# Kernel tuning notes

Measured on AMD Instinct MI355X. Metric: run time of the kernel, lower is better.

The kernel has to match this reference:

```python
import jax, jax.numpy as jnp
import numpy as np

B, S, D, H = 2, 2048, 2048, 16
HD = D // H
SCALE = 1.0 / np.sqrt(HD)


def setup_inputs() -> dict:
    key = jax.random.key(0)
    ks = jax.random.split(key, 11)
    xav = np.sqrt(6.0 / (D + D))  # xavier uniform bound for square weights
    def w(k):
        return jax.random.uniform(k, (D, D), jnp.float32, -xav, xav)
    return {
        "query": jax.random.normal(ks[0], (B, S, D), jnp.float32),
        "key": jax.random.normal(ks[1], (B, S, D), jnp.float32),
        "value": jax.random.normal(ks[2], (B, S, D), jnp.float32),
        "Wq": w(ks[3]), "bq": jnp.zeros((D,), jnp.float32),
        "Wk": w(ks[4]), "bk": jnp.zeros((D,), jnp.float32),
        "Wv": w(ks[5]), "bv": jnp.zeros((D,), jnp.float32),
        "Wo": w(ks[6]), "bo": jnp.zeros((D,), jnp.float32),
    }


def reference(query, key, value, Wq, bq, Wk, bk, Wv, bv, Wo, bo):
    # projections (torch Linear: x @ W.T + b)
    q = query @ Wq.T + bq
    k = key @ Wk.T + bk
    v = value @ Wv.T + bv
    # [B, H, S, HD]
    q = q.reshape(B, S, H, HD).transpose(0, 2, 1, 3)
    k = k.reshape(B, S, H, HD).transpose(0, 2, 1, 3)
    v = v.reshape(B, S, H, HD).transpose(0, 2, 1, 3)
    scores = jnp.einsum("bhqd,bhkd->bhqk", q, k) * SCALE
    causal = jnp.triu(jnp.ones((S, S), bool), k=1)
    scores = jnp.where(causal, -jnp.inf, scores)
    attn = jax.nn.softmax(scores, axis=-1)  # dropout p=0.0 -> identity
    out = jnp.einsum("bhqk,bhkd->bhqd", attn, v)
    out = out.transpose(0, 2, 1, 3).reshape(B, S, D)
    return out @ Wo.T + bo
```

## Files before the change

### kernel.cpp

```cpp
#include <hip/hip_runtime.h>
#include <hip/hip_bf16.h>


#define LOG2E 1.44269504088896340736f

typedef __attribute__((ext_vector_type(8))) short short8;
typedef __attribute__((ext_vector_type(4))) short short4b;
typedef __attribute__((ext_vector_type(4))) float floatx4;

__device__ __forceinline__ short f2bf(float f) {
  unsigned int u = __builtin_bit_cast(unsigned int, f);
  u += 0x7FFFu + ((u >> 16) & 1u);
  return (short)(u >> 16);
}

__device__ __forceinline__ short4b pack4bf(float a, float b, float c, float d) {
  __hip_bfloat162 lo = __float22bfloat162_rn(float2{a, b});
  __hip_bfloat162 hi = __float22bfloat162_rn(float2{c, d});
  short4b r;
  r[0] = __builtin_bit_cast(short, lo.x); r[1] = __builtin_bit_cast(short, lo.y);
  r[2] = __builtin_bit_cast(short, hi.x); r[3] = __builtin_bit_cast(short, hi.y);
  return r;
}

__device__ __forceinline__ void gl_lds16(const void* g, void* l) {
  __builtin_amdgcn_global_load_lds(
      (const __attribute__((address_space(1))) unsigned int*)g,
      (__attribute__((address_space(3))) unsigned int*)l, 16, 0, 0);
}

__global__ __launch_bounds__(256) void cvt_k(
    const float* __restrict__ s0, const float* __restrict__ s1,
    const float* __restrict__ s2, const float* __restrict__ s3,
    unsigned short* __restrict__ d0, unsigned short* __restrict__ d1,
    unsigned short* __restrict__ d2, unsigned short* __restrict__ d3, int n)
{
  const float* s; unsigned short* d;
  switch (blockIdx.y) {
    case 0: s = s0; d = d0; break;
    case 1: s = s1; d = d1; break;
    case 2: s = s2; d = d2; break;
    default: s = s3; d = d3; break;
  }
  const int i = (blockIdx.x * 256 + threadIdx.x) * 8;
  if (i >= n) return;
  float4 a = *(const float4*)(s + i);
  float4 b = *(const float4*)(s + i + 4);
  short8 v = (short8){f2bf(a.x), f2bf(a.y), f2bf(a.z), f2bf(a.w),
                      f2bf(b.x), f2bf(b.y), f2bf(b.z), f2bf(b.w)};
  *(short8*)(d + i) = v;
}

template<bool OUT_BF16, bool VT_OUT>
__global__ __launch_bounds__(512, 1) void gemm8_k(
    const unsigned short* __restrict__ A, const unsigned short* __restrict__ Bt,
    const float* __restrict__ bias, void* __restrict__ Cptr,
    int M, int N, int K, float alpha)
{
  __shared__ __align__(16) unsigned short As[3][256 * 64];
  __shared__ __align__(16) unsigned short Bs[3][128 * 64];
  (void)M;

  const int tid  = threadIdx.x;
  const int lane = tid & 63;
  const int wave = tid >> 6;
  const int quad = lane >> 4;
  const int l16  = lane & 15;
  const int lx7  = l16 & 7;
  const int wm   = wave >> 1, wn = wave & 1;

  int bx, by;
  if (gridDim.x == 16 && gridDim.y == 16) {
    const int lin  = (int)(blockIdx.y * 16 + blockIdx.x);
    const int xcd  = lin & 7;
    const int slot = lin >> 3;
    bx = (xcd & 1) * 8 + (slot & 7);
    by = (xcd >> 1) * 4 + (slot >> 3);
  } else { bx = (int)blockIdx.x; by = (int)blockIdx.y; }
  const long bm  = (long)by * 256;
  const long bn  = (long)bx * 128;

  const unsigned short* gA[4]; int lAo[4];
  const unsigned short* gB[2]; int lBo[2];
#pragma unroll
  for (int j = 0; j < 4; ++j) {
    const int pa = ((j >> 1) * 16 + wave * 2 + (j & 1)) * 64 + lane;
    const int r = pa >> 3, cp = pa & 7, cs = cp ^ (r & 7);
    gA[j]  = A + (bm + r) * (long)K + cs * 8;
    lAo[j] = pa * 8;
  }
#pragma unroll
  for (int j = 0; j < 2; ++j) {
    const int pb = (wave * 2 + j) * 64 + lane;
    const int r = pb >> 3, cp = pb & 7, cs = cp ^ (r & 7);
    gB[j]  = Bt + (bn + r) * (long)K + cs * 8;
    lBo[j] = pb * 8;
  }

  floatx4 acc[4][4];
#pragma unroll
  for (int i = 0; i < 4; ++i)
#pragma unroll
    for (int j = 0; j < 4; ++j) acc[i][j] = (floatx4){0.f, 0.f, 0.f, 0.f};

  const int NT = K >> 6;

#pragma unroll
  for (int j = 0; j < 4; ++j) gl_lds16(gA[j], &As[0][lAo[j]]);
#pragma unroll
  for (int j = 0; j < 2; ++j) gl_lds16(gB[j], &Bs[0][lBo[j]]);
  if (NT > 1) {
#pragma unroll
    for (int j = 0; j < 4; ++j) gl_lds16(gA[j] + 64, &As[1][lAo[j]]);
#pragma unroll
    for (int j = 0; j < 2; ++j) gl_lds16(gB[j] + 64, &Bs[1][lBo[j]]);
    asm volatile("s_waitcnt vmcnt(6)" ::: "memory");
  } else {
    asm volatile("s_waitcnt vmcnt(0)" ::: "memory");
  }
  __builtin_amdgcn_s_barrier();

  int cur = 0;
  for (int t = 0; t < NT; ++t) {
    int nx2 = cur + 2; if (nx2 >= 3) nx2 -= 3;
    const long kk2 = (long)(t + 2) * 64;
    const bool st  = (t + 2) < NT;
    const unsigned short* Ab = As[cur];
    const unsigned short* Bb = Bs[cur];

    short8 af[4][2];
#pragma unroll
    for (int mt = 0; mt < 4; ++mt)
#pragma unroll
      for (int ks = 0; ks < 2; ++ks)
        af[mt][ks] = *(const short8*)&Ab[(wm * 64 + mt * 16 + l16) * 64 +
                                         (((ks * 4 + quad) ^ lx7) * 8)];

    short8 bf00 = *(const short8*)&Bb[(wn * 64 +  0 + l16) * 64 + (((0 + quad) ^ lx7) * 8)];
    short8 bf01 = *(const short8*)&Bb[(wn * 64 +  0 + l16) * 64 + (((4 + quad) ^ lx7) * 8)];
    short8 bf10 = *(const short8*)&Bb[(wn * 64 + 16 + l16) * 64 + (((0 + quad) ^ lx7) * 8)];
    short8 bf11 = *(const short8*)&Bb[(wn * 64 + 16 + l16) * 64 + (((4 + quad) ^ lx7) * 8)];
    if (st) { gl_lds16(gA[0] + kk2, &As[nx2][lAo[0]]);
              gl_lds16(gA[1] + kk2, &As[nx2][lAo[1]]);
              gl_lds16(gA[2] + kk2, &As[nx2][lAo[2]]); }
    __builtin_amdgcn_s_barrier();
    asm volatile("s_waitcnt lgkmcnt(0)");
    __builtin_amdgcn_s_setprio(1);
#pragma unroll
    for (int mt = 0; mt < 4; ++mt) {
      acc[mt][0] = __builtin_amdgcn_mfma_f32_16x16x32_bf16(af[mt][0], bf00, acc[mt][0], 0, 0, 0);
      acc[mt][0] = __builtin_amdgcn_mfma_f32_16x16x32_bf16(af[mt][1], bf01, acc[mt][0], 0, 0, 0);
      acc[mt][1] = __builtin_amdgcn_mfma_f32_16x16x32_bf16(af[mt][0], bf10, acc[mt][1], 0, 0, 0);
      acc[mt][1] = __builtin_amdgcn_mfma_f32_16x16x32_bf16(af[mt][1], bf11, acc[mt][1], 0, 0, 0);
    }
    __builtin_amdgcn_s_setprio(0);
    __builtin_amdgcn_s_barrier();

    bf00 = *(const short8*)&Bb[(wn * 64 + 32 + l16) * 64 + (((0 + quad) ^ lx7) * 8)];
    bf01 = *(const short8*)&Bb[(wn * 64 + 32 + l16) * 64 + (((4 + quad) ^ lx7) * 8)];
    bf10 = *(const short8*)&Bb[(wn * 64 + 48 + l16) * 64 + (((0 + quad) ^ lx7) * 8)];
    bf11 = *(const short8*)&Bb[(wn * 64 + 48 + l16) * 64 + (((4 + quad) ^ lx7) * 8)];
    if (st) { gl_lds16(gA[3] + kk2, &As[nx2][lAo[3]]);
              gl_lds16(gB[0] + kk2, &Bs[nx2][lBo[0]]);
              gl_lds16(gB[1] + kk2, &Bs[nx2][lBo[1]]); }
    __builtin_amdgcn_s_barrier();
    asm volatile("s_waitcnt lgkmcnt(0)");
    __builtin_amdgcn_s_setprio(1);
#pragma unroll
    for (int mt = 0; mt < 4; ++mt) {
      acc[mt][2] = __builtin_amdgcn_mfma_f32_16x16x32_bf16(af[mt][0], bf00, acc[mt][2], 0, 0, 0);
      acc[mt][2] = __builtin_amdgcn_mfma_f32_16x16x32_bf16(af[mt][1], bf01, acc[mt][2], 0, 0, 0);
      acc[mt][3] = __builtin_amdgcn_mfma_f32_16x16x32_bf16(af[mt][0], bf10, acc[mt][3], 0, 0, 0);
      acc[mt][3] = __builtin_amdgcn_mfma_f32_16x16x32_bf16(af[mt][1], bf11, acc[mt][3], 0, 0, 0);
    }
    __builtin_amdgcn_s_setprio(0);
    if (t + 1 < NT) {
      if (st) asm volatile("s_waitcnt vmcnt(6)" ::: "memory");
      else    asm volatile("s_waitcnt vmcnt(0)" ::: "memory");
    }
    __builtin_amdgcn_s_barrier();

    cur = cur + 1 >= 3 ? 0 : cur + 1;
  }

  if (VT_OUT) {
    __syncthreads();
    unsigned short* Ct = &As[0][0];
#pragma unroll
    for (int nt = 0; nt < 4; ++nt) {
      const int col_l = wn * 64 + nt * 16 + l16;
      const float bval = bias[bn + col_l];
#pragma unroll
      for (int mt = 0; mt < 4; ++mt) {
        const int row_l = wm * 64 + mt * 16 + quad * 4;
#pragma unroll
        for (int rg = 0; rg < 4; ++rg)
          Ct[col_l * 264 + row_l + rg] = (unsigned short)f2bf((acc[mt][nt][rg] + bval) * alpha);
      }
    }
    __syncthreads();
    const int b  = (int)(bm >> 11);
    const int s0 = (int)(bm & 2047);
    const int d   = tid >> 2;
    const int seg = tid & 3;
    unsigned short* dst = (unsigned short*)Cptr +
        ((long)(b * 16 + bx) * 128 + d) * 2048 + s0 + seg * 64;
    const unsigned short* src = &Ct[d * 264 + seg * 64];
#pragma unroll
    for (int c = 0; c < 8; ++c)
      *(uint4*)(dst + c * 8) = *(const uint4*)(src + c * 8);
  } else {
#pragma unroll
    for (int nt = 0; nt < 4; ++nt) {
      const long col = bn + wn * 64 + nt * 16 + l16;
      const float bval = bias[col];
#pragma unroll
      for (int mt = 0; mt < 4; ++mt) {
#pragma unroll
        for (int rg = 0; rg < 4; ++rg) {
          const long row = bm + wm * 64 + mt * 16 + quad * 4 + rg;
          const float v = (acc[mt][nt][rg] + bval) * alpha;
          if (OUT_BF16) ((unsigned short*)Cptr)[row * (long)N + col] = (unsigned short)f2bf(v);
          else          ((float*)Cptr)[row * (long)N + col] = v;
        }
      }
    }
  }
}

template<bool A_BF16, bool OUT_BF16, bool VT_OUT>
__global__ __launch_bounds__(256, 2) void gemm_bias_k(
    const void* __restrict__ Aptr, const float* __restrict__ Bt,
    const float* __restrict__ bias, void* __restrict__ Cptr,
    int M, int N, int K, float alpha)
{
  __shared__ __align__(16) unsigned short smem[128 * 136];
  unsigned short* As = smem;
  unsigned short* Bs = smem + 128 * 40;

  const int tid  = threadIdx.x;
  const int lane = tid & 63;
  const int wave = tid >> 6;
  const int quad = lane >> 4;
  const int l16  = lane & 15;
  const int wr   = wave >> 1, wc = wave & 1;
  const long bm  = (long)blockIdx.y * 128;
  const long bn  = (long)blockIdx.x * 128;

  floatx4 acc[4][4];
#pragma unroll
  for (int i = 0; i < 4; ++i)
#pragma unroll
    for (int j = 0; j < 4; ++j) acc[i][j] = (floatx4){0.f, 0.f, 0.f, 0.f};

  const int srow = tid >> 2;
  const int cc   = tid & 3;

  for (int k0 = 0; k0 < K; k0 += 32) {
    __syncthreads();
#pragma unroll
    for (int r = 0; r < 2; ++r) {
      const int row = srow + r * 64;
      short8 av, bv;
      if (A_BF16) {
        av = *(const short8*)((const unsigned short*)Aptr + (bm + row) * (long)K + k0 + cc * 8);
      } else {
        const float* ap = (const float*)Aptr + (bm + row) * (long)K + k0 + cc * 8;
        float4 f0 = *(const float4*)ap;
        float4 f1 = *(const float4*)(ap + 4);
        av = (short8){f2bf(f0.x), f2bf(f0.y), f2bf(f0.z), f2bf(f0.w),
                      f2bf(f1.x), f2bf(f1.y), f2bf(f1.z), f2bf(f1.w)};
      }
      {
        const float* bp = Bt + (bn + row) * (long)K + k0 + cc * 8;
        float4 g0 = *(const float4*)bp;
        float4 g1 = *(const float4*)(bp + 4);
        bv = (short8){f2bf(g0.x), f2bf(g0.y), f2bf(g0.z), f2bf(g0.w),
                      f2bf(g1.x), f2bf(g1.y), f2bf(g1.z), f2bf(g1.w)};
      }
      *(short8*)&As[row * 40 + cc * 8] = av;
      *(short8*)&Bs[row * 40 + cc * 8] = bv;
    }
    __syncthreads();

    short8 af[4], bf[4];
#pragma unroll
    for (int t = 0; t < 4; ++t) {
      af[t] = *(const short8*)&As[(wr * 64 + t * 16 + l16) * 40 + quad * 8];
      bf[t] = *(const short8*)&Bs[(wc * 64 + t * 16 + l16) * 40 + quad * 8];
    }
#pragma unroll
    for (int mt = 0; mt < 4; ++mt)
#pragma unroll
      for (int nt = 0; nt < 4; ++nt)
        acc[mt][nt] = __builtin_amdgcn_mfma_f32_16x16x32_bf16(af[mt], bf[nt], acc[mt][nt], 0, 0, 0);
  }

  if (VT_OUT) {
    __syncthreads();
    unsigned short* Ct = smem;
#pragma unroll
    for (int nt = 0; nt < 4; ++nt) {
      const long col = bn + wc * 64 + nt * 16 + l16;
      const float bval = bias[col];
      const int col_l = wc * 64 + nt * 16 + l16;
#pragma unroll
      for (int mt = 0; mt < 4; ++mt) {
        const int row_l = wr * 64 + mt * 16 + quad * 4;
#pragma unroll
        for (int rg = 0; rg < 4; ++rg)
          Ct[col_l * 136 + row_l + rg] = (unsigned short)f2bf((acc[mt][nt][rg] + bval) * alpha);
      }
    }
    __syncthreads();
    const int b  = (int)(bm >> 11);
    const int s0 = (int)(bm & 2047);
    const int r    = tid >> 1;
    const int half = tid & 1;
    unsigned short* dst = (unsigned short*)Cptr +
        ((long)(b * 16 + blockIdx.x) * 128 + r) * 2048 + s0 + half * 64;
    const unsigned short* src = &Ct[r * 136 + half * 64];
#pragma unroll
    for (int c = 0; c < 8; ++c)
      *(uint4*)(dst + c * 8) = *(const uint4*)(src + c * 8);
  } else {
#pragma unroll
    for (int nt = 0; nt < 4; ++nt) {
      const long col = bn + wc * 64 + nt * 16 + l16;
      const float bval = bias[col];
#pragma unroll
      for (int mt = 0; mt < 4; ++mt) {
#pragma unroll
        for (int rg = 0; rg < 4; ++rg) {
          const long row = bm + wr * 64 + mt * 16 + quad * 4 + rg;
          const float v = (acc[mt][nt][rg] + bval) * alpha;
          if (OUT_BF16) ((unsigned short*)Cptr)[row * (long)N + col] = (unsigned short)f2bf(v);
          else          ((float*)Cptr)[row * (long)N + col] = v;
        }
      }
    }
  }
}

__global__ __launch_bounds__(256, 2) void flash_attn_k(
    const unsigned short* __restrict__ Q,
    const unsigned short* __restrict__ Kp,
    const unsigned short* __restrict__ Vt,
    unsigned short* __restrict__ O)
{
  constexpr int S = 2048, D = 2048, HD = 128;
  constexpr int PS = 72;

  __shared__ __align__(16) unsigned short Ks[2][64 * 128];
  __shared__ __align__(16) unsigned short Vst[2][128 * 64];
  __shared__ __align__(16) unsigned short Ps[64 * PS];

  const int tid  = threadIdx.x;
  const int lane = tid & 63;
  const int w    = tid >> 6;
  const int quad = lane >> 4;
  const int l16  = lane & 15;
  const int lx7  = l16 & 7;

  const int bx  = blockIdx.x;
  const int by  = blockIdx.y;
  const int idx = by * 2 + (bx >> 3);
  const int bh  = (bx & 7) * 4 + (idx >> 4);
  const int qsel = idx & 15;

  const long headoff = (long)(bh >> 4) * S * D + (long)(bh & 15) * HD;
  const long vtoff   = (long)bh * HD * S;

  const unsigned short* gK[4]; int oK[4];
  const unsigned short* gV[4]; int oV[4];
#pragma unroll
  for (int i = 0; i < 4; ++i) {
    const int p = (w * 4 + i) * 64 + lane;
    { const int r = p >> 4, cp = p & 15, c = cp ^ (r & 7);
      gK[i] = Kp + headoff + (long)r * D + c * 8;  oK[i] = p * 8; }
    { const int r = p >> 3, cp = p & 7, c = cp ^ (r & 7);
      gV[i] = Vt + vtoff + (long)r * S + c * 8;    oV[i] = p * 8; }
  }

#pragma unroll 1
  for (int half = 0; half < 2; ++half) {
    const int qt = half ? (31 - qsel) : qsel;
    const int qbase = qt * 64;
    const int qrow  = qbase + w * 16 + l16;
    const int qloc  = w * 16 + l16;

    short8 aq[4];
    {
      const unsigned short* qp = Q + headoff + (long)qrow * D;
#pragma unroll
      for (int ks = 0; ks < 4; ++ks)
        aq[ks] = *(const short8*)(qp + ks * 32 + quad * 8);
    }

    floatx4 o_acc[8];
#pragma unroll
    for (int t = 0; t < 8; ++t) o_acc[t] = (floatx4){0.f, 0.f, 0.f, 0.f};
    float m_i = -INFINITY, l_i = 0.f;

#pragma unroll
    for (int i = 0; i < 4; ++i) gl_lds16(gK[i], &Ks[0][oK[i]]);
#pragma unroll
    for (int i = 0; i < 4; ++i) gl_lds16(gV[i], &Vst[0][oV[i]]);

    for (int kt = 0; kt <= qt; ++kt) {
      const int cur = kt & 1;
      const int kbase = kt * 64;
      if (kt < qt) {
        const long kb = (long)(kt + 1) * 64;
        const int nb = cur ^ 1;
#pragma unroll
        for (int i = 0; i < 4; ++i) gl_lds16(gK[i] + kb * D, &Ks[nb][oK[i]]);
#pragma unroll
        for (int i = 0; i < 4; ++i) gl_lds16(gV[i] + kb, &Vst[nb][oV[i]]);
        asm volatile("s_waitcnt vmcnt(8)" ::: "memory");
      } else {
        asm volatile("s_waitcnt vmcnt(0)" ::: "memory");
      }
      __builtin_amdgcn_s_barrier();

      const unsigned short* Kb = &Ks[cur][0];
      const unsigned short* Vb = &Vst[cur][0];

      floatx4 sc[4];
#pragma unroll
      for (int nt = 0; nt < 4; ++nt) sc[nt] = (floatx4){0.f, 0.f, 0.f, 0.f};
      __builtin_amdgcn_s_setprio(1);
#pragma unroll
      for (int nt = 0; nt < 4; ++nt) {
        const int krow = nt * 16 + l16;
#pragma unroll
        for (int ks = 0; ks < 4; ++ks) {
          const int cp = (ks * 4 + quad) ^ lx7;
          short8 kf = *(const short8*)&Kb[krow * 128 + cp * 8];
          sc[nt] = __builtin_amdgcn_mfma_f32_16x16x32_bf16(kf, aq[ks], sc[nt], 0, 0, 0);
        }
      }
      __builtin_amdgcn_s_setprio(0);

      float sv[4][4];
      float rmax = -INFINITY;
      if (kt == qt) {
        const int kg0 = kbase + quad * 4;
#pragma unroll
        for (int nt = 0; nt < 4; ++nt)
#pragma unroll
          for (int rg = 0; rg < 4; ++rg) {
            float v = sc[nt][rg];
            if (kg0 + nt * 16 + rg > qrow) v = -INFINITY;
            sv[nt][rg] = v;
            rmax = fmaxf(rmax, v);
          }
      } else {
#pragma unroll
        for (int nt = 0; nt < 4; ++nt)
#pragma unroll
          for (int rg = 0; rg < 4; ++rg) {
            sv[nt][rg] = sc[nt][rg];
            rmax = fmaxf(rmax, sc[nt][rg]);
          }
      }
      rmax = fmaxf(rmax, __shfl_xor(rmax, 16));
      rmax = fmaxf(rmax, __shfl_xor(rmax, 32));

      float al = 1.0f;
      if (__any(rmax > m_i + 8.0f)) {
        const float mn = fmaxf(m_i, rmax);
        al = exp2f(m_i - mn);
        m_i = mn;
#pragma unroll
        for (int t = 0; t < 8; ++t)
#pragma unroll
          for (int rg = 0; rg < 4; ++rg) o_acc[t][rg] *= al;
      }

      float rsum = 0.f;
#pragma unroll
      for (int nt = 0; nt < 4; ++nt) {
        float p0 = exp2f(sv[nt][0] - m_i), p1 = exp2f(sv[nt][1] - m_i);
        float p2 = exp2f(sv[nt][2] - m_i), p3 = exp2f(sv[nt][3] - m_i);
        rsum += (p0 + p1) + (p2 + p3);
        *(short4b*)&Ps[qloc * PS + nt * 16 + quad * 4] = pack4bf(p0, p1, p2, p3);
      }
      rsum += __shfl_xor(rsum, 16);
      rsum += __shfl_xor(rsum, 32);
      l_i = l_i * al + rsum;

      short8 pf[2];
#pragma unroll
      for (int ks = 0; ks < 2; ++ks)
        pf[ks] = *(const short8*)&Ps[qloc * PS + ks * 32 + quad * 8];

      __builtin_amdgcn_s_setprio(1);
#pragma unroll
      for (int t = 0; t < 8; ++t) {
        const int drow = t * 16 + l16;
#pragma unroll
        for (int ks = 0; ks < 2; ++ks) {
          const int cp = (ks * 4 + quad) ^ lx7;
          short8 vf = *(const short8*)&Vb[drow * 64 + cp * 8];
          o_acc[t] = __builtin_amdgcn_mfma_f32_16x16x32_bf16(vf, pf[ks], o_acc[t], 0, 0, 0);
        }
      }
      __builtin_amdgcn_s_setprio(0);
      __builtin_amdgcn_s_barrier();
    }

    const float rl = 1.0f / l_i;
    unsigned short* op = O + headoff + (long)qrow * D;
#pragma unroll
    for (int t = 0; t < 8; ++t) {
      *(short4b*)(op + t * 16 + quad * 4) =
          pack4bf(o_acc[t][0] * rl, o_acc[t][1] * rl, o_acc[t][2] * rl, o_acc[t][3] * rl);
    }
  }
}

extern "C" void kernel_launch(void* const* d_in, const int* in_sizes, int n_in,
                              void* d_out, int out_size, void* d_ws, size_t ws_size,
                              hipStream_t stream) {
  const float* query = (const float*)d_in[0];
  const float* key_  = (const float*)d_in[1];
  const float* value = (const float*)d_in[2];
  const float* Wq = (const float*)d_in[3];
  const float* bq = (const float*)d_in[4];
  const float* Wk = (const float*)d_in[5];
  const float* bk = (const float*)d_in[6];
  const float* Wv = (const float*)d_in[7];
  const float* bv = (const float*)d_in[8];
  const float* Wo = (const float*)d_in[9];
  const float* bo = (const float*)d_in[10];
  float* out = (float*)d_out;

  constexpr int Bz = 2, S = 2048, D = 2048;
  constexpr int M = Bz * S;
  constexpr long NELEM = (long)M * D;
  constexpr long WELEM = (long)D * D;

  const float qscale = 0.08838834764831845f * LOG2E;
  dim3 gridG(D / 128, M / 128);
  dim3 gridG8(D / 128, M / 256);

  const size_t need_full = (size_t)(6 * NELEM + 4 * WELEM) * 2;

  if (ws_size >= need_full) {
    unsigned short* Qp  = (unsigned short*)d_ws;
    unsigned short* Kp  = Qp + NELEM;
    unsigned short* Vt  = Kp + NELEM;
    unsigned short* Xq  = Vt + NELEM;
    unsigned short* Xk  = Xq + NELEM;
    unsigned short* Xv  = Xk + NELEM;
    unsigned short* Wqb = Xv + NELEM;
    unsigned short* Wkb = Wqb + WELEM;
    unsigned short* Wvb = Wkb + WELEM;
    unsigned short* Wob = Wvb + WELEM;
    unsigned short* Oa  = Xq;

    cvt_k<<<dim3(NELEM / (8 * 256), 3), 256, 0, stream>>>(
        query, key_, value, value, Xq, Xk, Xv, Xv, (int)NELEM);
    cvt_k<<<dim3(WELEM / (8 * 256), 4), 256, 0, stream>>>(
        Wq, Wk, Wv, Wo, Wqb, Wkb, Wvb, Wob, (int)WELEM);

    gemm8_k<true, false><<<gridG8, 512, 0, stream>>>(Xq, Wqb, bq, Qp, M, D, D, qscale);
    gemm8_k<true, false><<<gridG8, 512, 0, stream>>>(Xk, Wkb, bk, Kp, M, D, D, 1.0f);
    gemm8_k<true, true ><<<gridG8, 512, 0, stream>>>(Xv, Wvb, bv, Vt, M, D, D, 1.0f);

    flash_attn_k<<<dim3(16, 32), 256, 0, stream>>>(Qp, Kp, Vt, Oa);

    gemm8_k<false, false><<<gridG8, 512, 0, stream>>>(Oa, Wob, bo, out, M, D, D, 1.0f);
  } else {
    unsigned short* Qp = (unsigned short*)d_ws;
    unsigned short* Kp = Qp + NELEM;
    unsigned short* Vt = Kp + NELEM;
    unsigned short* Oa = Vt + NELEM;

    gemm_bias_k<false, true, false><<<gridG, 256, 0, stream>>>(query, Wq, bq, Qp, M, D, D, qscale);
    gemm_bias_k<false, true, false><<<gridG, 256, 0, stream>>>(key_,  Wk, bk, Kp, M, D, D, 1.0f);
    gemm_bias_k<false, true, true ><<<gridG, 256, 0, stream>>>(value, Wv, bv, Vt, M, D, D, 1.0f);

    flash_attn_k<<<dim3(16, 32), 256, 0, stream>>>(Qp, Kp, Vt, Oa);

    gemm_bias_k<true, false, false><<<gridG, 256, 0, stream>>>(Oa, Wo, bo, out, M, D, D, 1.0f);
  }
}
```

Before: 424.8 us.

## Merge conversion kernels, simplify GEMM k-loop, defer softmax row-sum reductions

The two fp32-to-bf16 conversion launches become a single seven-slice kernel, with activation slices looping four times per block. The GEMM main loop now issues all six async global-to-LDS loads up front, then all A and B fragment reads, then all 32 MFMAs under one barrier. The old loop split this into two half-phases with extra barriers and lgkmcnt waits. In flash attention, the cross-lane max shuffles run only when a rescale happens, and the row-sum shuffles move out of the loop to a single reduction at the end. This raises register pressure for B fragments and can weaken interleaving of LDS reads with MFMAs.

```diff
diff --git a/kernel.cpp b/kernel.cpp
--- a/kernel.cpp
+++ b/kernel.cpp
@@ -29,26 +29,37 @@
       (__attribute__((address_space(3))) unsigned int*)l, 16, 0, 0);
 }
 
-__global__ __launch_bounds__(256) void cvt_k(
+__global__ __launch_bounds__(256) void cvt7_k(
     const float* __restrict__ s0, const float* __restrict__ s1,
     const float* __restrict__ s2, const float* __restrict__ s3,
+    const float* __restrict__ s4, const float* __restrict__ s5,
+    const float* __restrict__ s6,
     unsigned short* __restrict__ d0, unsigned short* __restrict__ d1,
-    unsigned short* __restrict__ d2, unsigned short* __restrict__ d3, int n)
+    unsigned short* __restrict__ d2, unsigned short* __restrict__ d3,
+    unsigned short* __restrict__ d4, unsigned short* __restrict__ d5,
+    unsigned short* __restrict__ d6, int nAct, int nW)
 {
-  const float* s; unsigned short* d;
+  const float* s; unsigned short* d; int n, iters;
   switch (blockIdx.y) {
-    case 0: s = s0; d = d0; break;
-    case 1: s = s1; d = d1; break;
-    case 2: s = s2; d = d2; break;
-    default: s = s3; d = d3; break;
-  }
-  const int i = (blockIdx.x * 256 + threadIdx.x) * 8;
-  if (i >= n) return;
-  float4 a = *(const float4*)(s + i);
-  float4 b = *(const float4*)(s + i + 4);
-  short8 v = (short8){f2bf(a.x), f2bf(a.y), f2bf(a.z), f2bf(a.w),
-                      f2bf(b.x), f2bf(b.y), f2bf(b.z), f2bf(b.w)};
-  *(short8*)(d + i) = v;
+    case 0: s = s0; d = d0; n = nAct; iters = 4; break;
+    case 1: s = s1; d = d1; n = nAct; iters = 4; break;
+    case 2: s = s2; d = d2; n = nAct; iters = 4; break;
+    case 3: s = s3; d = d3; n = nW;   iters = 1; break;
+    case 4: s = s4; d = d4; n = nW;   iters = 1; break;
+    case 5: s = s5; d = d5; n = nW;   iters = 1; break;
+    default: s = s6; d = d6; n = nW;  iters = 1; break;
+  }
+#pragma unroll 1
+  for (int c = 0; c < iters; ++c) {
+    const long i = ((long)(blockIdx.x + c * 2048) * 256 + threadIdx.x) * 8;
+    if (i < n) {
+      float4 a = *(const float4*)(s + i);
+      float4 b = *(const float4*)(s + i + 4);
+      short8 v = (short8){f2bf(a.x), f2bf(a.y), f2bf(a.z), f2bf(a.w),
+                          f2bf(b.x), f2bf(b.y), f2bf(b.z), f2bf(b.w)};
+      *(short8*)(d + i) = v;
+    }
+  }
 }
 
 template<bool OUT_BF16, bool VT_OUT>
@@ -120,67 +131,55 @@
   }
   __builtin_amdgcn_s_barrier();
 
-  int cur = 0;
+  int cur3 = 0;
   for (int t = 0; t < NT; ++t) {
-    int nx2 = cur + 2; if (nx2 >= 3) nx2 -= 3;
+    int nx2 = cur3 + 2; if (nx2 >= 3) nx2 -= 3;
     const long kk2 = (long)(t + 2) * 64;
-    const bool st  = (t + 2) < NT;
-    const unsigned short* Ab = As[cur];
-    const unsigned short* Bb = Bs[cur];
-
-    short8 af[4][2];
+    const bool st2 = (t + 2) < NT;
+    const bool st1 = (t + 1) < NT;
+    const unsigned short* Ab = As[cur3];
+    const unsigned short* Bb = Bs[cur3];
+
+    if (st2) {
+      gl_lds16(gA[0] + kk2, &As[nx2][lAo[0]]);
+      gl_lds16(gA[1] + kk2, &As[nx2][lAo[1]]);
+      gl_lds16(gA[2] + kk2, &As[nx2][lAo[2]]);
+      gl_lds16(gA[3] + kk2, &As[nx2][lAo[3]]);
+      gl_lds16(gB[0] + kk2, &Bs[nx2][lBo[0]]);
+      gl_lds16(gB[1] + kk2, &Bs[nx2][lBo[1]]);
+    }
+
+    short8 af[4][2], bf[4][2];
 #pragma unroll
     for (int mt = 0; mt < 4; ++mt)
 #pragma unroll
       for (int ks = 0; ks < 2; ++ks)
         af[mt][ks] = *(const short8*)&Ab[(wm * 64 + mt * 16 + l16) * 64 +
                                          (((ks * 4 + quad) ^ lx7) * 8)];
-
-    short8 bf00 = *(const short8*)&Bb[(wn * 64 +  0 + l16) * 64 + (((0 + quad) ^ lx7) * 8)];
-    short8 bf01 = *(const short8*)&Bb[(wn * 64 +  0 + l16) * 64 + (((4 + quad) ^ lx7) * 8)];
-    short8 bf10 = *(const short8*)&Bb[(wn * 64 + 16 + l16) * 64 + (((0 + quad) ^ lx7) * 8)];
-    short8 bf11 = *(const short8*)&Bb[(wn * 64 + 16 + l16) * 64 + (((4 + quad) ^ lx7) * 8)];
-    if (st) { gl_lds16(gA[0] + kk2, &As[nx2][lAo[0]]);
-              gl_lds16(gA[1] + kk2, &As[nx2][lAo[1]]);
-              gl_lds16(gA[2] + kk2, &As[nx2][lAo[2]]); }
+#pragma unroll
+    for (int nt = 0; nt < 4; ++nt)
+#pragma unroll
+      for (int ks = 0; ks < 2; ++ks)
+        bf[nt][ks] = *(const short8*)&Bb[(wn * 64 + nt * 16 + l16) * 64 +
+                                         (((ks * 4 + quad) ^ lx7) * 8)];
+
+    __builtin_amdgcn_s_setprio(1);
+#pragma unroll
+    for (int nt = 0; nt < 4; ++nt)
+#pragma unroll
+      for (int mt = 0; mt < 4; ++mt) {
+        acc[mt][nt] = __builtin_amdgcn_mfma_f32_16x16x32_bf16(af[mt][0], bf[nt][0], acc[mt][nt], 0, 0, 0);
+        acc[mt][nt] = __builtin_amdgcn_mfma_f32_16x16x32_bf16(af[mt][1], bf[nt][1], acc[mt][nt], 0, 0, 0);
+      }
+    __builtin_amdgcn_s_setprio(0);
+
+    if (st1) {
+      if (st2) asm volatile("s_waitcnt vmcnt(6)" ::: "memory");
+      else     asm volatile("s_waitcnt vmcnt(0)" ::: "memory");
+    }
     __builtin_amdgcn_s_barrier();
-    asm volatile("s_waitcnt lgkmcnt(0)");
-    __builtin_amdgcn_s_setprio(1);
-#pragma unroll
-    for (int mt = 0; mt < 4; ++mt) {
-      acc[mt][0] = __builtin_amdgcn_mfma_f32_16x16x32_bf16(af[mt][0], bf00, acc[mt][0], 0, 0, 0);
-      acc[mt][0] = __builtin_amdgcn_mfma_f32_16x16x32_bf16(af[mt][1], bf01, acc[mt][0], 0, 0, 0);
-      acc[mt][1] = __builtin_amdgcn_mfma_f32_16x16x32_bf16(af[mt][0], bf10, acc[mt][1], 0, 0, 0);
-      acc[mt][1] = __builtin_amdgcn_mfma_f32_16x16x32_bf16(af[mt][1], bf11, acc[mt][1], 0, 0, 0);
-    }
-    __builtin_amdgcn_s_setprio(0);
-    __builtin_amdgcn_s_barrier();
-
-    bf00 = *(const short8*)&Bb[(wn * 64 + 32 + l16) * 64 + (((0 + quad) ^ lx7) * 8)];
-    bf01 = *(const short8*)&Bb[(wn * 64 + 32 + l16) * 64 + (((4 + quad) ^ lx7) * 8)];
-    bf10 = *(const short8*)&Bb[(wn * 64 + 48 + l16) * 64 + (((0 + quad) ^ lx7) * 8)];
-    bf11 = *(const short8*)&Bb[(wn * 64 + 48 + l16) * 64 + (((4 + quad) ^ lx7) * 8)];
-    if (st) { gl_lds16(gA[3] + kk2, &As[nx2][lAo[3]]);
-              gl_lds16(gB[0] + kk2, &Bs[nx2][lBo[0]]);
-              gl_lds16(gB[1] + kk2, &Bs[nx2][lBo[1]]); }
-    __builtin_amdgcn_s_barrier();
-    asm volatile("s_waitcnt lgkmcnt(0)");
-    __builtin_amdgcn_s_setprio(1);
-#pragma unroll
-    for (int mt = 0; mt < 4; ++mt) {
-      acc[mt][2] = __builtin_amdgcn_mfma_f32_16x16x32_bf16(af[mt][0], bf00, acc[mt][2], 0, 0, 0);
-      acc[mt][2] = __builtin_amdgcn_mfma_f32_16x16x32_bf16(af[mt][1], bf01, acc[mt][2], 0, 0, 0);
-      acc[mt][3] = __builtin_amdgcn_mfma_f32_16x16x32_bf16(af[mt][0], bf10, acc[mt][3], 0, 0, 0);
-      acc[mt][3] = __builtin_amdgcn_mfma_f32_16x16x32_bf16(af[mt][1], bf11, acc[mt][3], 0, 0, 0);
-    }
-    __builtin_amdgcn_s_setprio(0);
-    if (t + 1 < NT) {
-      if (st) asm volatile("s_waitcnt vmcnt(6)" ::: "memory");
-      else    asm volatile("s_waitcnt vmcnt(0)" ::: "memory");
-    }
-    __builtin_amdgcn_s_barrier();
-
-    cur = cur + 1 >= 3 ? 0 : cur + 1;
+
+    cur3 = cur3 + 1 >= 3 ? 0 : cur3 + 1;
   }
 
   if (VT_OUT) {
@@ -400,7 +399,8 @@
     floatx4 o_acc[8];
 #pragma unroll
     for (int t = 0; t < 8; ++t) o_acc[t] = (floatx4){0.f, 0.f, 0.f, 0.f};
-    float m_i = -INFINITY, l_i = 0.f;
+    float m_i = -INFINITY;
+    float l_p = 0.f;
 
 #pragma unroll
     for (int i = 0; i < 4; ++i) gl_lds16(gK[i], &Ks[0][oK[i]]);
@@ -443,7 +443,7 @@
       __builtin_amdgcn_s_setprio(0);
 
       float sv[4][4];
-      float rmax = -INFINITY;
+      float lmax = -INFINITY;
       if (kt == qt) {
         const int kg0 = kbase + quad * 4;
 #pragma unroll
@@ -453,7 +453,7 @@
             float v = sc[nt][rg];
             if (kg0 + nt * 16 + rg > qrow) v = -INFINITY;
             sv[nt][rg] = v;
-            rmax = fmaxf(rmax, v);
+            lmax = fmaxf(lmax, v);
           }
       } else {
 #pragma unroll
@@ -461,14 +461,14 @@
 #pragma unroll
           for (int rg = 0; rg < 4; ++rg) {
             sv[nt][rg] = sc[nt][rg];
-            rmax = fmaxf(rmax, sc[nt][rg]);
+            lmax = fmaxf(lmax, sc[nt][rg]);
           }
       }
-      rmax = fmaxf(rmax, __shfl_xor(rmax, 16));
-      rmax = fmaxf(rmax, __shfl_xor(rmax, 32));
 
       float al = 1.0f;
-      if (__any(rmax > m_i + 8.0f)) {
+      if (__any(lmax > m_i + 8.0f)) {
+        float rmax = fmaxf(lmax, __shfl_xor(lmax, 16));
+        rmax = fmaxf(rmax, __shfl_xor(rmax, 32));
         const float mn = fmaxf(m_i, rmax);
         al = exp2f(m_i - mn);
         m_i = mn;
@@ -486,9 +486,7 @@
         rsum += (p0 + p1) + (p2 + p3);
         *(short4b*)&Ps[qloc * PS + nt * 16 + quad * 4] = pack4bf(p0, p1, p2, p3);
       }
-      rsum += __shfl_xor(rsum, 16);
-      rsum += __shfl_xor(rsum, 32);
-      l_i = l_i * al + rsum;
+      l_p = l_p * al + rsum;
 
       short8 pf[2];
 #pragma unroll
@@ -510,6 +508,8 @@
       __builtin_amdgcn_s_barrier();
     }
 
+    float l_i = l_p + __shfl_xor(l_p, 16);
+    l_i += __shfl_xor(l_i, 32);
     const float rl = 1.0f / l_i;
     unsigned short* op = O + headoff + (long)qrow * D;
 #pragma unroll
@@ -560,10 +560,9 @@
     unsigned short* Wob = Wvb + WELEM;
     unsigned short* Oa  = Xq;
 
-    cvt_k<<<dim3(NELEM / (8 * 256), 3), 256, 0, stream>>>(
-        query, key_, value, value, Xq, Xk, Xv, Xv, (int)NELEM);
-    cvt_k<<<dim3(WELEM / (8 * 256), 4), 256, 0, stream>>>(
-        Wq, Wk, Wv, Wo, Wqb, Wkb, Wvb, Wob, (int)WELEM);
+    cvt7_k<<<dim3(2048, 7), 256, 0, stream>>>(
+        query, key_, value, Wq, Wk, Wv, Wo,
+        Xq, Xk, Xv, Wqb, Wkb, Wvb, Wob, (int)NELEM, (int)WELEM);
 
     gemm8_k<true, false><<<gridG8, 512, 0, stream>>>(Xq, Wqb, bq, Qp, M, D, D, qscale);
     gemm8_k<true, false><<<gridG8, 512, 0, stream>>>(Xk, Wkb, bk, Kp, M, D, D, 1.0f);
```

Result: slower. 450.0 us (+5.9%).
